# Kernel optimization log

Measured on AMD Instinct MI355X. Metric: run time of the kernel, lower is better.

## Reference

```python
import jax, jax.numpy as jnp
import numpy as np

B, S, E = 4096, 200, 128
ATT_H, MLP_H = 128, 256


def _glorot(key, shape):
    fan_in, fan_out = shape[0], shape[1]
    lim = np.sqrt(6.0 / (fan_in + fan_out)).astype(np.float32)
    return jax.random.uniform(key, shape, jnp.float32, -lim, lim)


def setup_inputs() -> dict:
    key = jax.random.key(0)
    ks = jax.random.split(key, 10)
    return {
        "behavior_emb": jax.random.normal(ks[0], (B, S, E), jnp.float32),
        "candidate_emb": jax.random.normal(ks[1], (B, E), jnp.float32),
        "fc1_w": _glorot(ks[2], (2 * E, ATT_H)),
        "fc1_b": jnp.zeros((ATT_H,), jnp.float32),
        "fc2_w": _glorot(ks[3], (ATT_H, 1)),
        "fc2_b": jnp.zeros((1,), jnp.float32),
        "mlp1_w": _glorot(ks[4], (2 * E, MLP_H)),
        "mlp1_b": jnp.zeros((MLP_H,), jnp.float32),
        "mlp2_w": _glorot(ks[5], (MLP_H, 1)),
        "mlp2_b": jnp.zeros((1,), jnp.float32),
    }


def reference(behavior_emb, candidate_emb, fc1_w, fc1_b, fc2_w, fc2_b,
              mlp1_w, mlp1_b, mlp2_w, mlp2_b):
    # Attention unit: split fc1 weight so we avoid materializing the concat.
    # concat([beh, cand]) @ fc1_w == beh @ W_b + cand @ W_c
    W_b, W_c = fc1_w[:E], fc1_w[E:]
    h = jax.nn.relu(jnp.einsum('bse,eh->bsh', behavior_emb, W_b)
                    + (candidate_emb @ W_c)[:, None, :] + fc1_b)  # [B,S,H]
    scores = jnp.einsum('bsh,h->bs', h, fc2_w[:, 0]) + fc2_b[0]   # [B,S]
    attn = jax.nn.softmax(scores, axis=-1)                         # [B,S]
    user_interest = jnp.einsum('bse,bs->be', behavior_emb, attn)   # [B,E]
    # MLP head
    x = jnp.concatenate([user_interest, candidate_emb], axis=1)    # [B,2E]
    z = jax.nn.relu(x @ mlp1_w + mlp1_b)
    logit = (z @ mlp2_w + mlp2_b)[:, 0]                            # [B]
    return logit
```

## Files before the change

### kernel.cpp

```cpp
#include <hip/hip_runtime.h>
#include <hip/hip_bf16.h>
#include <stdint.h>

#define BN   4096
#define SN   200
#define SPAD 224
#define EN   128
#define HN   128

typedef __attribute__((ext_vector_type(8)))  short  short8;
typedef __attribute__((ext_vector_type(16))) float  floatx16;

__device__ __forceinline__ unsigned short f2bf(float f) {
  union { float f; uint32_t u; } c; c.f = f;
  uint32_t r = c.u + 0x7fffu + ((c.u >> 16) & 1u);
  return (unsigned short)(r >> 16);
}
__device__ __forceinline__ float bf2f(unsigned short h) {
  union { uint32_t u; float f; } c; c.u = ((uint32_t)h) << 16;
  return c.f;
}
__device__ __forceinline__ float bcast_lane(float v, int l) {
  return __builtin_bit_cast(float, __builtin_amdgcn_readlane(__builtin_bit_cast(int, v), l));
}

__device__ __forceinline__ int aoff(int s, int g) {
  return s * 256 + (((g ^ (s & 15)) << 4));
}

__global__ __launch_bounds__(256, 2)
void din_main(const float* __restrict__ behavior, const float* __restrict__ cand,
              const float* __restrict__ fc1w, const float* __restrict__ fc1b,
              const float* __restrict__ fc2w, float* __restrict__ ws_ui) {
  __shared__ unsigned short Abuf[SPAD * EN];
  __shared__ float scores_s[SPAD];
  __shared__ float cvec[HN];
  __shared__ float w2s[HN];
  __shared__ float cand_s[EN];
  __shared__ float ui_s[EN];

  const int tid = threadIdx.x;
  const int b   = blockIdx.x;

  if (tid < SPAD) scores_s[tid] = 0.f;
  if (tid < EN) {
    cand_s[tid] = cand[(size_t)b * EN + tid];
    w2s[tid]    = fc2w[tid];
    ui_s[tid]   = 0.f;
  }
  __syncthreads();

  {
    const float* src = behavior + (size_t)b * SN * EN;
    #pragma unroll
    for (int it = 0; it < 28; ++it) {
      int q  = it * 256 + tid;
      int s  = q >> 5;
      int e4 = (q & 31) << 2;
      float4 v = make_float4(0.f, 0.f, 0.f, 0.f);
      if (s < SN) v = *(const float4*)(src + s * EN + e4);
      uint32_t p0 = (uint32_t)f2bf(v.x) | ((uint32_t)f2bf(v.y) << 16);
      uint32_t p1 = (uint32_t)f2bf(v.z) | ((uint32_t)f2bf(v.w) << 16);
      char* dst = (char*)Abuf + s * 256 + ((((e4 >> 3) ^ (s & 15))) << 4) + ((e4 & 7) << 1);
      *(uint2*)dst = make_uint2(p0, p1);
    }
  }

  if (tid < HN) {
    float a = fc1b[tid];
    for (int e = 0; e < EN; ++e)
      a = fmaf(cand_s[e], fc1w[(EN + e) * HN + tid], a);
    cvec[tid] = a;
  }
  __syncthreads();

  const int wv   = tid >> 6;
  const int lane = tid & 63;
  const int half = lane >> 5;
  const int l31  = lane & 31;

  const int hcol = wv * 32 + l31;
  short8 afr[8];
  #pragma unroll
  for (int t = 0; t < 8; ++t) {
    #pragma unroll
    for (int j = 0; j < 8; ++j) {
      int e = t * 16 + half * 8 + j;
      afr[t][j] = (short)f2bf(fc1w[e * HN + hcol]);
    }
  }
  float cadd[16], wmul[16];
  #pragma unroll
  for (int r = 0; r < 16; ++r) {
    int hr = wv * 32 + (r & 3) + ((r >> 2) << 3) + (half << 2);
    cadd[r] = cvec[hr];
    wmul[r] = w2s[hr];
  }

  for (int st = 0; st < 7; ++st) {
    floatx16 acc = {0.f,0.f,0.f,0.f,0.f,0.f,0.f,0.f,0.f,0.f,0.f,0.f,0.f,0.f,0.f,0.f};
    const int srow = st * 32 + l31;
    #pragma unroll
    for (int t = 0; t < 8; ++t) {
      int g = 2 * t + half;
      const short8 bfr = *(const short8*)((const char*)Abuf + aoff(srow, g));
      acc = __builtin_amdgcn_mfma_f32_32x32x16_bf16(afr[t], bfr, acc, 0, 0, 0);
    }
    float part = 0.f;
    #pragma unroll
    for (int r = 0; r < 16; ++r) {
      float h = fmaxf(acc[r] + cadd[r], 0.f);
      part = fmaf(h, wmul[r], part);
    }
    part += __shfl_xor(part, 32, 64);
    if (lane < 32) atomicAdd(&scores_s[st * 32 + l31], part);
  }
  __syncthreads();

  if (wv == 0) {
    float v0[4];
    #pragma unroll
    for (int k = 0; k < 4; ++k) {
      int s = k * 64 + lane;
      v0[k] = (s < SN) ? scores_s[s] : -3.0e38f;
    }
    float m = fmaxf(fmaxf(v0[0], v0[1]), fmaxf(v0[2], v0[3]));
    #pragma unroll
    for (int off = 32; off >= 1; off >>= 1) m = fmaxf(m, __shfl_xor(m, off, 64));
    float e0[4], sum = 0.f;
    #pragma unroll
    for (int k = 0; k < 4; ++k) { e0[k] = __expf(v0[k] - m); sum += e0[k]; }
    #pragma unroll
    for (int off = 32; off >= 1; off >>= 1) sum += __shfl_xor(sum, off, 64);
    float inv = 1.0f / sum;
    #pragma unroll
    for (int k = 0; k < 4; ++k) {
      int s = k * 64 + lane;
      if (s < SN) scores_s[s] = e0[k] * inv;
    }
  }
  __syncthreads();

  {
    const int ec = (tid & 15) << 3;
    const int sg = tid >> 4;
    float ua[8] = {0.f,0.f,0.f,0.f,0.f,0.f,0.f,0.f};
    for (int s = sg; s < SN; s += 16) {
      float a = scores_s[s];
      const short8 bv = *(const short8*)((const char*)Abuf + aoff(s, ec >> 3));
      #pragma unroll
      for (int j = 0; j < 8; ++j) ua[j] = fmaf(a, bf2f((unsigned short)bv[j]), ua[j]);
    }
    #pragma unroll
    for (int j = 0; j < 8; ++j) atomicAdd(&ui_s[ec + j], ua[j]);
  }
  __syncthreads();
  if (tid < EN) ws_ui[(size_t)b * EN + tid] = ui_s[tid];
}

__global__ __launch_bounds__(256, 2)
void din_mlp(const float* __restrict__ ws_ui, const float* __restrict__ cand,
             const float* __restrict__ w1, const float* __restrict__ b1,
             const float* __restrict__ w2, const float* __restrict__ b2,
             float* __restrict__ out) {
  const int tid  = threadIdx.x;
  const int lane = tid & 63;
  const int wv   = tid >> 6;
  const int r0   = blockIdx.x * 8;

  float xr[8][4];
  #pragma unroll
  for (int r = 0; r < 8; ++r) {
    #pragma unroll
    for (int c = 0; c < 4; ++c) {
      int i = c * 64 + lane;
      int row = r0 + r;
      xr[r][c] = (i < 128) ? ws_ui[row * 128 + i] : cand[row * 128 + (i - 128)];
    }
  }

  const int j = tid;
  float acc[8];
  const float bj = b1[j];
  #pragma unroll
  for (int r = 0; r < 8; ++r) acc[r] = bj;

  #pragma unroll
  for (int c = 0; c < 4; ++c) {
    #pragma unroll 8
    for (int il = 0; il < 64; ++il) {
      float w = w1[(c * 64 + il) * 256 + j];
      #pragma unroll
      for (int r = 0; r < 8; ++r)
        acc[r] = fmaf(bcast_lane(xr[r][c], il), w, acc[r]);
    }
  }

  const float w2j = w2[j];
  float part[8];
  #pragma unroll
  for (int r = 0; r < 8; ++r) part[r] = fmaxf(acc[r], 0.f) * w2j;
  #pragma unroll
  for (int off = 32; off >= 1; off >>= 1) {
    #pragma unroll
    for (int r = 0; r < 8; ++r) part[r] += __shfl_xor(part[r], off, 64);
  }

  __shared__ float red[4][8];
  if (lane == 0) {
    #pragma unroll
    for (int r = 0; r < 8; ++r) red[wv][r] = part[r];
  }
  __syncthreads();
  if (tid < 8)
    out[r0 + tid] = red[0][tid] + red[1][tid] + red[2][tid] + red[3][tid] + b2[0];
}

extern "C" void kernel_launch(void* const* d_in, const int* in_sizes, int n_in,
                              void* d_out, int out_size, void* d_ws, size_t ws_size,
                              hipStream_t stream) {
  const float* behavior = (const float*)d_in[0];
  const float* cand     = (const float*)d_in[1];
  const float* fc1w     = (const float*)d_in[2];
  const float* fc1b     = (const float*)d_in[3];
  const float* fc2w     = (const float*)d_in[4];
  const float* m1w      = (const float*)d_in[6];
  const float* m1b      = (const float*)d_in[7];
  const float* m2w      = (const float*)d_in[8];
  const float* m2b      = (const float*)d_in[9];
  float* outp  = (float*)d_out;
  float* ws_ui = (float*)d_ws;

  din_main<<<BN, 256, 0, stream>>>(behavior, cand, fc1w, fc1b, fc2w, ws_ui);
  din_mlp<<<BN / 8, 256, 0, stream>>>(ws_ui, cand, m1w, m1b, m2w, m2b, outp);
}
```

Before: 683.0 us.

## Precompute bf16 weight fragments, shrink LDS, split loads, raise occupancy

Adds a prep kernel that converts the fc1 behavior-weight fragments to bf16 once per call, so each block stops reconverting them. The main kernel drops the padded rows from LDS and raises launch bounds to 3 blocks per CU. It issues behavior loads in two register batches overlapped with the cvec GEMV, which is now split across all 256 threads. Score reads clamp out-of-range rows, and the user-interest reduction adds wave shuffles before the LDS atomics. The MLP kernel handles 4 rows per block for more blocks; the added register pressure could cause spills.

```diff
diff --git a/kernel.cpp b/kernel.cpp
--- a/kernel.cpp
+++ b/kernel.cpp
@@ -4,7 +4,6 @@
 
 #define BN   4096
 #define SN   200
-#define SPAD 224
 #define EN   128
 #define HN   128
 
@@ -28,49 +27,39 @@
   return s * 256 + (((g ^ (s & 15)) << 4));
 }
 
-__global__ __launch_bounds__(256, 2)
+__global__ void din_prep(const float* __restrict__ fc1w, short8* __restrict__ ws_afr) {
+  const int t    = blockIdx.x & 7;
+  const int wv   = blockIdx.x >> 3;
+  const int lane = threadIdx.x;
+  const int half = lane >> 5;
+  const int hcol = wv * 32 + (lane & 31);
+  short8 fr;
+  #pragma unroll
+  for (int j = 0; j < 8; ++j) {
+    int e = t * 16 + half * 8 + j;
+    fr[j] = (short)f2bf(fc1w[e * HN + hcol]);
+  }
+  ws_afr[((wv * 8 + t) << 6) + lane] = fr;
+}
+
+__global__ __launch_bounds__(256, 3)
 void din_main(const float* __restrict__ behavior, const float* __restrict__ cand,
               const float* __restrict__ fc1w, const float* __restrict__ fc1b,
-              const float* __restrict__ fc2w, float* __restrict__ ws_ui) {
-  __shared__ unsigned short Abuf[SPAD * EN];
-  __shared__ float scores_s[SPAD];
-  __shared__ float cvec[HN];
-  __shared__ float w2s[HN];
+              const float* __restrict__ fc2w, const short8* __restrict__ ws_afr,
+              float* __restrict__ ws_ui) {
+  __shared__ unsigned short Abuf[SN * EN];
+  __shared__ float scores_s[SN];
+  __shared__ float cvec2[2][HN];
   __shared__ float cand_s[EN];
   __shared__ float ui_s[EN];
 
   const int tid = threadIdx.x;
   const int b   = blockIdx.x;
 
-  if (tid < SPAD) scores_s[tid] = 0.f;
+  if (tid < SN) scores_s[tid] = 0.f;
   if (tid < EN) {
     cand_s[tid] = cand[(size_t)b * EN + tid];
-    w2s[tid]    = fc2w[tid];
     ui_s[tid]   = 0.f;
-  }
-  __syncthreads();
-
-  {
-    const float* src = behavior + (size_t)b * SN * EN;
-    #pragma unroll
-    for (int it = 0; it < 28; ++it) {
-      int q  = it * 256 + tid;
-      int s  = q >> 5;
-      int e4 = (q & 31) << 2;
-      float4 v = make_float4(0.f, 0.f, 0.f, 0.f);
-      if (s < SN) v = *(const float4*)(src + s * EN + e4);
-      uint32_t p0 = (uint32_t)f2bf(v.x) | ((uint32_t)f2bf(v.y) << 16);
-      uint32_t p1 = (uint32_t)f2bf(v.z) | ((uint32_t)f2bf(v.w) << 16);
-      char* dst = (char*)Abuf + s * 256 + ((((e4 >> 3) ^ (s & 15))) << 4) + ((e4 & 7) << 1);
-      *(uint2*)dst = make_uint2(p0, p1);
-    }
-  }
-
-  if (tid < HN) {
-    float a = fc1b[tid];
-    for (int e = 0; e < EN; ++e)
-      a = fmaf(cand_s[e], fc1w[(EN + e) * HN + tid], a);
-    cvec[tid] = a;
   }
   __syncthreads();
 
@@ -79,31 +68,70 @@
   const int half = lane >> 5;
   const int l31  = lane & 31;
 
-  const int hcol = wv * 32 + l31;
+  const float* src = behavior + (size_t)b * SN * EN;
+  float4 va[13];
+  #pragma unroll
+  for (int u = 0; u < 13; ++u) {
+    int q = u * 256 + tid;
+    va[u] = *(const float4*)(src + (q >> 5) * EN + ((q & 31) << 2));
+  }
   short8 afr[8];
   #pragma unroll
-  for (int t = 0; t < 8; ++t) {
-    #pragma unroll
-    for (int j = 0; j < 8; ++j) {
-      int e = t * 16 + half * 8 + j;
-      afr[t][j] = (short)f2bf(fc1w[e * HN + hcol]);
-    }
-  }
+  for (int t = 0; t < 8; ++t) afr[t] = ws_afr[((wv * 8 + t) << 6) + lane];
+
+  {
+    const int h  = tid & 127;
+    const int eh = tid >> 7;
+    float p0 = (eh == 0) ? fc1b[h] : 0.f, p1 = 0.f;
+    const float* wc = fc1w + (size_t)(EN + eh * 64) * HN + h;
+    #pragma unroll 8
+    for (int e = 0; e < 64; e += 2) {
+      p0 = fmaf(cand_s[eh * 64 + e],     wc[(size_t)e * HN],       p0);
+      p1 = fmaf(cand_s[eh * 64 + e + 1], wc[(size_t)(e + 1) * HN], p1);
+    }
+    cvec2[eh][h] = p0 + p1;
+  }
+
+  #pragma unroll
+  for (int u = 0; u < 13; ++u) {
+    int q = u * 256 + tid, s = q >> 5, e4 = (q & 31) << 2;
+    uint32_t p0 = (uint32_t)f2bf(va[u].x) | ((uint32_t)f2bf(va[u].y) << 16);
+    uint32_t p1 = (uint32_t)f2bf(va[u].z) | ((uint32_t)f2bf(va[u].w) << 16);
+    char* dst = (char*)Abuf + s * 256 + ((((e4 >> 3) ^ (s & 15))) << 4) + ((e4 & 7) << 1);
+    *(uint2*)dst = make_uint2(p0, p1);
+  }
+  float4 vb[12];
+  #pragma unroll
+  for (int u = 0; u < 12; ++u) {
+    int q = (u + 13) * 256 + tid;
+    vb[u] = *(const float4*)(src + (q >> 5) * EN + ((q & 31) << 2));
+  }
+  #pragma unroll
+  for (int u = 0; u < 12; ++u) {
+    int q = (u + 13) * 256 + tid, s = q >> 5, e4 = (q & 31) << 2;
+    uint32_t p0 = (uint32_t)f2bf(vb[u].x) | ((uint32_t)f2bf(vb[u].y) << 16);
+    uint32_t p1 = (uint32_t)f2bf(vb[u].z) | ((uint32_t)f2bf(vb[u].w) << 16);
+    char* dst = (char*)Abuf + s * 256 + ((((e4 >> 3) ^ (s & 15))) << 4) + ((e4 & 7) << 1);
+    *(uint2*)dst = make_uint2(p0, p1);
+  }
+  __syncthreads();
+
   float cadd[16], wmul[16];
   #pragma unroll
   for (int r = 0; r < 16; ++r) {
     int hr = wv * 32 + (r & 3) + ((r >> 2) << 3) + (half << 2);
-    cadd[r] = cvec[hr];
-    wmul[r] = w2s[hr];
+    cadd[r] = cvec2[0][hr] + cvec2[1][hr];
+    wmul[r] = fc2w[hr];
   }
 
   for (int st = 0; st < 7; ++st) {
     floatx16 acc = {0.f,0.f,0.f,0.f,0.f,0.f,0.f,0.f,0.f,0.f,0.f,0.f,0.f,0.f,0.f,0.f};
     const int srow = st * 32 + l31;
+    const int sr   = (srow < SN) ? srow : (SN - 1);
     #pragma unroll
     for (int t = 0; t < 8; ++t) {
       int g = 2 * t + half;
-      const short8 bfr = *(const short8*)((const char*)Abuf + aoff(srow, g));
+      const short8 bfr = *(const short8*)((const char*)Abuf + aoff(sr, g));
       acc = __builtin_amdgcn_mfma_f32_32x32x16_bf16(afr[t], bfr, acc, 0, 0, 0);
     }
     float part = 0.f;
@@ -113,7 +141,7 @@
       part = fmaf(h, wmul[r], part);
     }
     part += __shfl_xor(part, 32, 64);
-    if (lane < 32) atomicAdd(&scores_s[st * 32 + l31], part);
+    if (lane < 32 && srow < SN) atomicAdd(&scores_s[srow], part);
   }
   __syncthreads();
 
@@ -142,23 +170,30 @@
   __syncthreads();
 
   {
-    const int ec = (tid & 15) << 3;
+    const int g  = tid & 15;
     const int sg = tid >> 4;
     float ua[8] = {0.f,0.f,0.f,0.f,0.f,0.f,0.f,0.f};
     for (int s = sg; s < SN; s += 16) {
       float a = scores_s[s];
-      const short8 bv = *(const short8*)((const char*)Abuf + aoff(s, ec >> 3));
+      const short8 bv = *(const short8*)((const char*)Abuf + aoff(s, g));
       #pragma unroll
       for (int j = 0; j < 8; ++j) ua[j] = fmaf(a, bf2f((unsigned short)bv[j]), ua[j]);
     }
     #pragma unroll
-    for (int j = 0; j < 8; ++j) atomicAdd(&ui_s[ec + j], ua[j]);
+    for (int j = 0; j < 8; ++j) {
+      ua[j] += __shfl_xor(ua[j], 16, 64);
+      ua[j] += __shfl_xor(ua[j], 32, 64);
+    }
+    if (lane < 16) {
+      #pragma unroll
+      for (int j = 0; j < 8; ++j) atomicAdd(&ui_s[(g << 3) + j], ua[j]);
+    }
   }
   __syncthreads();
   if (tid < EN) ws_ui[(size_t)b * EN + tid] = ui_s[tid];
 }
 
-__global__ __launch_bounds__(256, 2)
+__global__ __launch_bounds__(256, 4)
 void din_mlp(const float* __restrict__ ws_ui, const float* __restrict__ cand,
              const float* __restrict__ w1, const float* __restrict__ b1,
              const float* __restrict__ w2, const float* __restrict__ b2,
@@ -166,11 +201,11 @@
   const int tid  = threadIdx.x;
   const int lane = tid & 63;
   const int wv   = tid >> 6;
-  const int r0   = blockIdx.x * 8;
-
-  float xr[8][4];
-  #pragma unroll
-  for (int r = 0; r < 8; ++r) {
+  const int r0   = blockIdx.x * 4;
+
+  float xr[4][4];
+  #pragma unroll
+  for (int r = 0; r < 4; ++r) {
     #pragma unroll
     for (int c = 0; c < 4; ++c) {
       int i = c * 64 + lane;
@@ -180,10 +215,8 @@
   }
 
   const int j = tid;
-  float acc[8];
   const float bj = b1[j];
-  #pragma unroll
-  for (int r = 0; r < 8; ++r) acc[r] = bj;
+  float acc[4] = {bj, bj, bj, bj};
 
   #pragma unroll
   for (int c = 0; c < 4; ++c) {
@@ -191,28 +224,28 @@
     for (int il = 0; il < 64; ++il) {
       float w = w1[(c * 64 + il) * 256 + j];
       #pragma unroll
-      for (int r = 0; r < 8; ++r)
+      for (int r = 0; r < 4; ++r)
         acc[r] = fmaf(bcast_lane(xr[r][c], il), w, acc[r]);
     }
   }
 
   const float w2j = w2[j];
-  float part[8];
-  #pragma unroll
-  for (int r = 0; r < 8; ++r) part[r] = fmaxf(acc[r], 0.f) * w2j;
+  float part[4];
+  #pragma unroll
+  for (int r = 0; r < 4; ++r) part[r] = fmaxf(acc[r], 0.f) * w2j;
   #pragma unroll
   for (int off = 32; off >= 1; off >>= 1) {
     #pragma unroll
-    for (int r = 0; r < 8; ++r) part[r] += __shfl_xor(part[r], off, 64);
-  }
-
-  __shared__ float red[4][8];
+    for (int r = 0; r < 4; ++r) part[r] += __shfl_xor(part[r], off, 64);
+  }
+
+  __shared__ float red[4][4];
   if (lane == 0) {
     #pragma unroll
-    for (int r = 0; r < 8; ++r) red[wv][r] = part[r];
-  }
-  __syncthreads();
-  if (tid < 8)
+    for (int r = 0; r < 4; ++r) red[wv][r] = part[r];
+  }
+  __syncthreads();
+  if (tid < 4)
     out[r0 + tid] = red[0][tid] + red[1][tid] + red[2][tid] + red[3][tid] + b2[0];
 }
 
@@ -230,7 +263,9 @@
   const float* m2b      = (const float*)d_in[9];
   float* outp  = (float*)d_out;
   float* ws_ui = (float*)d_ws;
-
-  din_main<<<BN, 256, 0, stream>>>(behavior, cand, fc1w, fc1b, fc2w, ws_ui);
-  din_mlp<<<BN / 8, 256, 0, stream>>>(ws_ui, cand, m1w, m1b, m2w, m2b, outp);
-}
+  short8* ws_afr = (short8*)((char*)d_ws + (size_t)BN * EN * 4);
+
+  din_prep<<<32, 64, 0, stream>>>(fc1w, ws_afr);
+  din_main<<<BN, 256, 0, stream>>>(behavior, cand, fc1w, fc1b, fc2w, ws_afr, ws_ui);
+  din_mlp<<<BN / 4, 256, 0, stream>>>(ws_ui, cand, m1w, m1b, m2w, m2b, outp);
+}
```

After: 620.5 us. -9.1%, faster.
